# Kernel tuning notes

Hardware: AMD Instinct MI355X
Metric: run time of the kernel (lower is better)

The kernel has to match this reference:

```python
import jax, jax.numpy as jnp
import numpy as np

K = 20
EPS = 1e-5
NEG_SLOPE = 0.2


def knn_idx(feat, k):
    # feat: (B, N, C). Pairwise neg squared distance, top-k nearest (self included).
    inner = jnp.einsum('bnc,bmc->bnm', feat, feat)          # (B,N,N)
    sq = jnp.sum(feat * feat, axis=-1)                      # (B,N)
    pd = 2.0 * inner - sq[:, :, None] - sq[:, None, :]      # -||xi-xj||^2
    return jax.lax.top_k(pd, k)[1]                          # (B,N,k)


def edge_conv(feat, W, g, b, m, v, k):
    # feat: (B,N,C); W: (O, 2C); BN params over O channels (eval-mode BN).
    idx = knn_idx(feat, k)                                  # (B,N,k)
    nbr = jnp.take_along_axis(feat[:, None, :, :], idx[..., None], axis=2)  # (B,N,k,C)
    ctr = jnp.broadcast_to(feat[:, :, None, :], nbr.shape)
    edge = jnp.concatenate([nbr - ctr, ctr], axis=-1)       # (B,N,k,2C)
    h = jnp.einsum('bnkc,oc->bnko', edge, W)                # 1x1 conv
    h = (h - m) * (g / jnp.sqrt(v + EPS)) + b               # BatchNorm2d (eval)
    h = jnp.where(h >= 0, h, NEG_SLOPE * h)                 # LeakyReLU(0.2)
    return jnp.max(h, axis=2)                               # max over k -> (B,N,O)


def setup_inputs() -> dict:
    key = jax.random.key(0)
    ks = jax.random.split(key, 21)
    B, N, C = 4, 4096, 3
    d = {'x': jax.random.normal(ks[0], (B, N, C), dtype=jnp.float32)}
    dims = [(64, 2 * 3), (64, 2 * 64), (128, 2 * 64), (256, 2 * 128)]
    for i, (o, c) in enumerate(dims, start=1):
        j = 1 + (i - 1) * 5
        d[f'W{i}'] = jax.random.normal(ks[j], (o, c), dtype=jnp.float32) * (1.0 / np.sqrt(c))
        d[f'g{i}'] = jax.random.uniform(ks[j + 1], (o,), minval=0.5, maxval=1.5, dtype=jnp.float32)
        d[f'b{i}'] = jax.random.normal(ks[j + 2], (o,), dtype=jnp.float32) * 0.1
        d[f'm{i}'] = jax.random.normal(ks[j + 3], (o,), dtype=jnp.float32) * 0.1
        d[f'v{i}'] = jax.random.uniform(ks[j + 4], (o,), minval=0.5, maxval=1.5, dtype=jnp.float32)
    return d


def reference(x, W1, g1, b1, m1, v1, W2, g2, b2, m2, v2,
              W3, g3, b3, m3, v3, W4, g4, b4, m4, v4):
    x1 = edge_conv(x, W1, g1, b1, m1, v1, K)    # (B,N,64)
    x2 = edge_conv(x1, W2, g2, b2, m2, v2, K)   # (B,N,64)
    x3 = edge_conv(x2, W3, g3, b3, m3, v3, K)   # (B,N,128)
    x4 = edge_conv(x3, W4, g4, b4, m4, v4, K)   # (B,N,256)
    return x4
```

## Files before the change

kernel.cpp:

```cpp
#include <hip/hip_runtime.h>

#define NTOT 4096
#define NBATCH 4
#define KNN 20
#define JSPLIT 8
#define KMRG 28
#define CSLOTM 512

constexpr float NEG_INF = -3.0e38f;

typedef __attribute__((ext_vector_type(8))) short bf16x8;
typedef __attribute__((ext_vector_type(4))) float f32x4;

__device__ __forceinline__ unsigned pk(float f, int j) {
  unsigned u = __float_as_uint(f);
  u = (u & 0x80000000u) ? ~u : (u | 0x80000000u);
  return (u & 0xFFFFF000u) | (unsigned)j;
}

__device__ __forceinline__ void pins8(unsigned u, unsigned (&tv)[8]) {
  if (u > tv[0]) {
    tv[0] = u;
#pragma unroll
    for (int x = 1; x < 8; x++) {
      unsigned mn = min(tv[0], tv[x]);
      unsigned mx = max(tv[0], tv[x]);
      tv[0] = mn;
      tv[x] = mx;
    }
  }
}

__device__ __forceinline__ void gll16(const void* g, void* l) {
  __builtin_amdgcn_global_load_lds(
      (const __attribute__((address_space(1))) unsigned int*)g,
      (__attribute__((address_space(3))) unsigned int*)l, 16, 0, 0);
}

__global__ void prep_w(const float* __restrict__ W, const float* __restrict__ gg,
                       const float* __restrict__ bb, const float* __restrict__ mm,
                       const float* __restrict__ vv, float* __restrict__ Wc,
                       float* __restrict__ bias, int O, int C) {
  int t = blockIdx.x * 256 + threadIdx.x;
  if (t >= 2 * O * C) return;
  int o2 = t / C, c = t - o2 * C;
  int o = (o2 < O) ? o2 : o2 - O;
  float s = gg[o] * rsqrtf(vv[o] + 1e-5f);
  float w = (o2 < O) ? W[o * 2 * C + c] * s
                     : (W[o * 2 * C + C + c] - W[o * 2 * C + c]) * s;
  Wc[o2 * C + c] = w;
  if (o2 >= O && c == 0) bias[o] = bb[o] - mm[o] * s;
}

__global__ void cvt_k(const float* __restrict__ f, ushort* __restrict__ hi,
                      ushort* __restrict__ lo) {
  int p = blockIdx.x * 256 + threadIdx.x;
  float x = f[p];
  unsigned u = __float_as_uint(x);
  unsigned h = (u + 0x7FFFu + ((u >> 16) & 1u)) >> 16;
  float hf = __uint_as_float(h << 16);
  float r = x - hf;
  unsigned v = __float_as_uint(r);
  unsigned l = (v + 0x7FFFu + ((v >> 16) & 1u)) >> 16;
  hi[p] = (ushort)h;
  lo[p] = (ushort)l;
}

__global__ void cvt3_k(const float* __restrict__ f, ushort* __restrict__ hi,
                       ushort* __restrict__ lo) {
  int p = blockIdx.x * 256 + threadIdx.x;
  int pt = p >> 5, dim = p & 31;
  float x = (dim < 3) ? f[pt * 3 + dim] : 0.f;
  unsigned u = __float_as_uint(x);
  unsigned h = (u + 0x7FFFu + ((u >> 16) & 1u)) >> 16;
  float hf = __uint_as_float(h << 16);
  float r = x - hf;
  unsigned v = __float_as_uint(r);
  unsigned l = (v + 0x7FFFu + ((v >> 16) & 1u)) >> 16;
  hi[p] = (ushort)h;
  lo[p] = (ushort)l;
}

template <int C>
__global__ void sqh_k(const float* __restrict__ f, float* __restrict__ sqh) {
  int p = blockIdx.x * 256 + threadIdx.x;
  const float* r = f + (size_t)p * C;
  float s = 0.f;
#pragma unroll
  for (int c4 = 0; c4 < C / 4; c4++) {
    float4 v = *(const float4*)&r[c4 * 4];
    s += v.x * v.x + v.y * v.y + v.z * v.z + v.w * v.w;
  }
  sqh[p] = 0.5f * s;
}

__global__ void sqh3_k(const float* __restrict__ f, float* __restrict__ sqh) {
  int p = blockIdx.x * 256 + threadIdx.x;
  float a = f[(size_t)p * 3 + 0];
  float b2 = f[(size_t)p * 3 + 1];
  float c = f[(size_t)p * 3 + 2];
  sqh[p] = 0.5f * (a * a + b2 * b2 + c * c);
}

template <int C>
__global__ __launch_bounds__(512, 4) void knn_m(const ushort* __restrict__ Xhi,
                                                const ushort* __restrict__ Xlo,
                                                const float* __restrict__ sqh,
                                                unsigned* __restrict__ cval) {
  constexpr int NK = C / 32;
  constexpr int NJT = NTOT / (128 * JSPLIT);
  __shared__ __align__(16) char smem[67584];
  float* sqB = (float*)(smem + 65536);

  int tid = threadIdx.x;
  int raw = blockIdx.x;
  int b = raw & 3;
  int js = (raw >> 3) & (JSPLIT - 1);
  int it = (((raw >> 6) & 15) << 1) | ((raw >> 2) & 1);
  int i0 = it * 128;
  const ushort* xh = Xhi + (size_t)b * NTOT * C;
  const ushort* xl = Xlo + (size_t)b * NTOT * C;

  int l = tid & 63, wid = tid >> 6;
  int wi = wid & 3, wj = wid >> 2;
  int n = l & 15, quad = l >> 4;
  int xr16 = (n & 7) << 4;

  int t0 = l & 1, t1 = (l >> 1) & 1, t2 = (l >> 2) & 1, t3 = (l >> 3) & 1,
      t4 = (l >> 4) & 1, t5 = (l >> 5) & 1;
  int Rl = (t2 ^ t4) | (t3 << 1) | (t4 << 2) | (t5 << 3);
  int ql = (t0 ^ t2 ^ t4) | ((t1 ^ t3) << 1);

  int jbase = js * (NTOT / JSPLIT);

  if (tid < 128) {
    float4 s4 = *(const float4*)&sqh[b * NTOT + jbase + tid * 4];
    *(float4*)&sqB[tid * 4] = s4;
  }
  __syncthreads();

  unsigned tv[2][8];
#pragma unroll
  for (int ti = 0; ti < 2; ti++)
#pragma unroll
    for (int x = 0; x < 8; x++) tv[ti][x] = 0u;

  auto issue = [&](int jtn, int kcn, char* buf) {
    int j0n = jbase + jtn * 128;
    int R = Rl + wid * 16;
    size_t gA = (size_t)(i0 + R) * C + kcn + ql * 8;
    size_t gB = (size_t)(j0n + R) * C + kcn + ql * 8;
    char* ld = buf + wid * 1024;
    gll16(xh + gA, ld);
    gll16(xl + gA, ld + 8192);
    gll16(xh + gB, ld + 16384);
    gll16(xl + gB, ld + 24576);
  };

  issue(0, 0, smem);

  int g = 0;
  for (int jt = 0; jt < NJT; jt++) {
    int j0 = jbase + jt * 128;

    f32x4 acc[4][2];
#pragma unroll
    for (int tj = 0; tj < 4; tj++)
#pragma unroll
      for (int ti = 0; ti < 2; ti++) acc[tj][ti] = (f32x4)(0.f);

    for (int kc = 0; kc < NK; kc++) {
      __builtin_amdgcn_s_barrier();
      int njt = (kc + 1 < NK) ? jt : ((jt + 1 == NJT) ? 0 : jt + 1);
      int nkc = (kc + 1 < NK) ? (kc + 1) * 32 : 0;
      issue(njt, nkc, smem + ((g + 1) & 1) * 32768);
      asm volatile("s_waitcnt vmcnt(4)" ::: "memory");
      __builtin_amdgcn_s_barrier();
      const char* bc = smem + (g & 1) * 32768;

      bf16x8 ah[2], al_[2];
#pragma unroll
      for (int ti = 0; ti < 2; ti++) {
        int row = wi * 32 + ti * 16 + n;
        int off = (row * 64 + quad * 16) ^ xr16;
        ah[ti] = *(const bf16x8*)(bc + off);
        al_[ti] = *(const bf16x8*)(bc + 8192 + off);
      }
#pragma unroll
      for (int tj = 0; tj < 4; tj++) {
        int row = wj * 64 + tj * 16 + n;
        int off = (row * 64 + quad * 16) ^ xr16;
        bf16x8 bh = *(const bf16x8*)(bc + 16384 + off);
        bf16x8 bl = *(const bf16x8*)(bc + 24576 + off);
#pragma unroll
        for (int ti = 0; ti < 2; ti++) {
          acc[tj][ti] = __builtin_amdgcn_mfma_f32_16x16x32_bf16(bh, ah[ti], acc[tj][ti], 0, 0, 0);
          acc[tj][ti] = __builtin_amdgcn_mfma_f32_16x16x32_bf16(bh, al_[ti], acc[tj][ti], 0, 0, 0);
          acc[tj][ti] = __builtin_amdgcn_mfma_f32_16x16x32_bf16(bl, ah[ti], acc[tj][ti], 0, 0, 0);
        }
      }
      g++;
    }

    float4 sq4[4];
#pragma unroll
    for (int tj = 0; tj < 4; tj++)
      sq4[tj] = *(const float4*)&sqB[jt * 128 + wj * 64 + tj * 16 + quad * 4];
#pragma unroll
    for (int ti = 0; ti < 2; ti++) {
#pragma unroll
      for (int tj = 0; tj < 4; tj++) {
        float v0 = acc[tj][ti][0] - sq4[tj].x;
        float v1 = acc[tj][ti][1] - sq4[tj].y;
        float v2 = acc[tj][ti][2] - sq4[tj].z;
        float v3 = acc[tj][ti][3] - sq4[tj].w;
        float m4 = fmaxf(fmaxf(v0, v1), fmaxf(v2, v3));
        if (pk(m4, 0xFFF) > tv[ti][0]) {
          int jb = j0 + wj * 64 + tj * 16 + quad * 4;
          pins8(pk(v0, jb + 0), tv[ti]);
          pins8(pk(v1, jb + 1), tv[ti]);
          pins8(pk(v2, jb + 2), tv[ti]);
          pins8(pk(v3, jb + 3), tv[ti]);
        }
      }
    }
  }

#pragma unroll
  for (int ti = 0; ti < 2; ti++) {
    int p = b * NTOT + i0 + wi * 32 + ti * 16 + n;
    unsigned* dst = cval + (size_t)p * CSLOTM + js * 64 + wj * 32 + quad * 8;
    uint4 o0, o1;
    o0.x = tv[ti][0]; o0.y = tv[ti][1]; o0.z = tv[ti][2]; o0.w = tv[ti][3];
    o1.x = tv[ti][4]; o1.y = tv[ti][5]; o1.z = tv[ti][6]; o1.w = tv[ti][7];
    *(uint4*)&dst[0] = o0;
    *(uint4*)&dst[4] = o1;
  }
}

template <int C, int NC>
__global__ __launch_bounds__(256) void kref_w(const float* __restrict__ feat,
                                              const unsigned* __restrict__ cval,
                                              int* __restrict__ outidx) {
  constexpr int NPL = NC / 64;
  int tid = threadIdx.x;
  int lane = tid & 63;
  int p = blockIdx.x * 4 + (tid >> 6);
  int b = p >> 12;
  int i = p & (NTOT - 1);
  const float* fb = feat + (size_t)b * NTOT * C;

  unsigned c[NPL];
  if constexpr (NPL == 8) {
    uint4 aa = *(const uint4*)&cval[(size_t)p * NC + lane * 8];
    uint4 bb2 = *(const uint4*)&cval[(size_t)p * NC + lane * 8 + 4];
    c[0] = aa.x; c[1] = aa.y; c[2] = aa.z; c[3] = aa.w;
    c[4] = bb2.x; c[5] = bb2.y; c[6] = bb2.z; c[7] = bb2.w;
  } else {
    uint4 aa = *(const uint4*)&cval[(size_t)p * NC + lane * 4];
    c[0] = aa.x; c[1] = aa.y; c[2] = aa.z; c[3] = aa.w;
  }

  int myj = -1;
#pragma unroll
  for (int t = 0; t < KMRG; t++) {
    unsigned m = c[0];
#pragma unroll
    for (int x = 1; x < NPL; x++) m = max(m, c[x]);
#pragma unroll
    for (int s = 1; s < 64; s <<= 1) m = max(m, (unsigned)__shfl_xor((int)m, s));
    if (lane == t) myj = (int)(m & 0xFFFu);
#pragma unroll
    for (int x = 0; x < NPL; x++)
      if (c[x] == m) c[x] = 0;
  }

  float myval = NEG_INF;
  if constexpr (C == 3) {
    if (lane < KMRG) {
      float x0 = fb[(size_t)i * 3 + 0];
      float x1 = fb[(size_t)i * 3 + 1];
      float x2 = fb[(size_t)i * 3 + 2];
      float y0 = fb[(size_t)myj * 3 + 0];
      float y1 = fb[(size_t)myj * 3 + 1];
      float y2 = fb[(size_t)myj * 3 + 2];
      float d0 = x0 - y0, d1 = x1 - y1, d2 = x2 - y2;
      myval = -(d0 * d0 + d1 * d1 + d2 * d2);
    }
  } else {
    constexpr int SL = C / 8;
    int m8 = lane & 7;
    float4 xs[SL / 4];
#pragma unroll
    for (int q4 = 0; q4 < SL / 4; q4++)
      xs[q4] = *(const float4*)&fb[(size_t)i * C + m8 * SL + q4 * 4];
#pragma unroll
    for (int ps = 0; ps < (KMRG + 7) / 8; ps++) {
      int src = ps * 8 + (lane >> 3);
      src = (src < KMRG) ? src : KMRG - 1;
      int j = __shfl(myj, src);
      float d = 0.f;
#pragma unroll
      for (int q4 = 0; q4 < SL / 4; q4++) {
        float4 yv = *(const float4*)&fb[(size_t)j * C + m8 * SL + q4 * 4];
        float dx = xs[q4].x - yv.x;
        float dy = xs[q4].y - yv.y;
        float dz = xs[q4].z - yv.z;
        float dw = xs[q4].w - yv.w;
        d += dx * dx + dy * dy + dz * dz + dw * dw;
      }
#pragma unroll
      for (int s = 1; s < 8; s <<= 1) d += __shfl_xor(d, s);
      float sd = __shfl(d, (lane & 7) << 3);
      bool upd = ((lane >> 3) == ps) && (lane < KMRG);
      myval = upd ? -sd : myval;
    }
  }

#pragma unroll
  for (int k = 2; k <= 64; k <<= 1) {
#pragma unroll
    for (int j2 = k >> 1; j2 > 0; j2 >>= 1) {
      float ov = __shfl_xor(myval, j2);
      int oj = __shfl_xor(myj, j2);
      bool ogt = (ov > myval) || (ov == myval && oj < myj);
      bool lower = ((lane & j2) == 0);
      bool desc = ((lane & k) == 0);
      bool take = (desc == (lower == ogt));
      myval = take ? ov : myval;
      myj = take ? oj : myj;
    }
  }

  if (lane < KNN) outidx[(size_t)p * KNN + lane] = myj;
}

__global__ __launch_bounds__(256) void gemm128(const float* __restrict__ A,
                                               const float* __restrict__ Wc,
                                               const float* __restrict__ bias,
                                               float* __restrict__ Y, int K, int N2,
                                               int O) {
  constexpr int P = 140;
  __shared__ float As[16 * P];
  __shared__ float Bs[16 * P];
  int tid = threadIdx.x;
  int n0 = blockIdx.x * 128;
  int m0 = blockIdx.y * 128;
  int tx = tid & 15, ty = tid >> 4;
  int aoff = (ty * 8) + (((ty * 8) >> 5) << 2);
  int boff = (tx * 8) + (((tx * 8) >> 5) << 2);
  float acc[8][8];
#pragma unroll
  for (int ii = 0; ii < 8; ii++)
#pragma unroll
    for (int jj = 0; jj < 8; jj++) acc[ii][jj] = 0.f;

  for (int kc = 0; kc < K; kc += 16) {
    __syncthreads();
#pragma unroll
    for (int l = 0; l < 2; l++) {
      int e = tid + 256 * l;
      int rr = e >> 2, c4 = e & 3;
      int sc = rr + ((rr >> 5) << 2);
      float4 va = *(const float4*)&A[(size_t)(m0 + rr) * K + kc + c4 * 4];
      As[(c4 * 4 + 0) * P + sc] = va.x;
      As[(c4 * 4 + 1) * P + sc] = va.y;
      As[(c4 * 4 + 2) * P + sc] = va.z;
      As[(c4 * 4 + 3) * P + sc] = va.w;
      float4 vb = *(const float4*)&Wc[(size_t)(n0 + rr) * K + kc + c4 * 4];
      Bs[(c4 * 4 + 0) * P + sc] = vb.x;
      Bs[(c4 * 4 + 1) * P + sc] = vb.y;
      Bs[(c4 * 4 + 2) * P + sc] = vb.z;
      Bs[(c4 * 4 + 3) * P + sc] = vb.w;
    }
    __syncthreads();
#pragma unroll 8
    for (int k = 0; k < 16; k++) {
      float4 a0 = *(const float4*)&As[k * P + aoff];
      float4 a1 = *(const float4*)&As[k * P + aoff + 4];
      float4 b0 = *(const float4*)&Bs[k * P + boff];
      float4 b1 = *(const float4*)&Bs[k * P + boff + 4];
      float av[8] = {a0.x, a0.y, a0.z, a0.w, a1.x, a1.y, a1.z, a1.w};
      float bv[8] = {b0.x, b0.y, b0.z, b0.w, b1.x, b1.y, b1.z, b1.w};
#pragma unroll
      for (int ii = 0; ii < 8; ii++)
#pragma unroll
        for (int jj = 0; jj < 8; jj++)
          acc[ii][jj] = fmaf(av[ii], bv[jj], acc[ii][jj]);
    }
  }

  int col0 = n0 + tx * 8;
  float bv[8];
#pragma unroll
  for (int jj = 0; jj < 8; jj++) {
    int col = col0 + jj;
    bv[jj] = (col >= O) ? bias[col - O] : 0.f;
  }
#pragma unroll
  for (int ii = 0; ii < 8; ii++) {
    int row = m0 + ty * 8 + ii;
    float4 o0, o1;
    o0.x = acc[ii][0] + bv[0];
    o0.y = acc[ii][1] + bv[1];
    o0.z = acc[ii][2] + bv[2];
    o0.w = acc[ii][3] + bv[3];
    o1.x = acc[ii][4] + bv[4];
    o1.y = acc[ii][5] + bv[5];
    o1.z = acc[ii][6] + bv[6];
    o1.w = acc[ii][7] + bv[7];
    *(float4*)&Y[(size_t)row * N2 + col0] = o0;
    *(float4*)&Y[(size_t)row * N2 + col0 + 4] = o1;
  }
}

__global__ __launch_bounds__(256) void gemm_k(const float* __restrict__ A,
                                              const float* __restrict__ Wc,
                                              const float* __restrict__ bias,
                                              float* __restrict__ Y, int K, int N2,
                                              int O) {
  __shared__ float As[8 * 68];
  __shared__ float Bs[8 * 68];
  int tid = threadIdx.x;
  int n0 = blockIdx.x * 64;
  int m0 = blockIdx.y * 64;
  int tx = tid & 15, ty = tid >> 4;
  float acc[4][4] = {};
  for (int k0 = 0; k0 < K; k0 += 8) {
    __syncthreads();
    {
      int e = tid, mm = e >> 3, kk = e & 7;
      As[kk * 68 + mm] = (k0 + kk < K) ? A[(size_t)(m0 + mm) * K + k0 + kk] : 0.f;
      int nn = mm;
      Bs[kk * 68 + nn] = (k0 + kk < K) ? Wc[(size_t)(n0 + nn) * K + k0 + kk] : 0.f;
      e = tid + 256;
      mm = e >> 3;
      kk = e & 7;
      As[kk * 68 + mm] = (k0 + kk < K) ? A[(size_t)(m0 + mm) * K + k0 + kk] : 0.f;
      nn = mm;
      Bs[kk * 68 + nn] = (k0 + kk < K) ? Wc[(size_t)(n0 + nn) * K + k0 + kk] : 0.f;
    }
    __syncthreads();
#pragma unroll
    for (int kk = 0; kk < 8; kk++) {
      float4 av = *(float4*)&As[kk * 68 + ty * 4];
      float4 bv = *(float4*)&Bs[kk * 68 + tx * 4];
      float a[4] = {av.x, av.y, av.z, av.w};
      float bb2[4] = {bv.x, bv.y, bv.z, bv.w};
#pragma unroll
      for (int ii = 0; ii < 4; ii++)
#pragma unroll
        for (int jj = 0; jj < 4; jj++) acc[ii][jj] += a[ii] * bb2[jj];
    }
  }
  int col = n0 + tx * 4;
  bool isV = (col >= O);
  float b0 = 0.f, b1 = 0.f, b2 = 0.f, b3 = 0.f;
  if (isV) {
    b0 = bias[col + 0 - O];
    b1 = bias[col + 1 - O];
    b2 = bias[col + 2 - O];
    b3 = bias[col + 3 - O];
  }
#pragma unroll
  for (int ii = 0; ii < 4; ii++) {
    int row = m0 + ty * 4 + ii;
    float4 o4;
    o4.x = acc[ii][0] + b0;
    o4.y = acc[ii][1] + b1;
    o4.z = acc[ii][2] + b2;
    o4.w = acc[ii][3] + b3;
    *(float4*)&Y[(size_t)row * N2 + col] = o4;
  }
}

template <int O>
__global__ __launch_bounds__(256) void gmax_v(const float* __restrict__ Y,
                                              const int* __restrict__ idx,
                                              float* __restrict__ out) {
  constexpr int T = O / 4;
  constexpr int G = 256 / T;
  int tid = threadIdx.x;
  int p = blockIdx.x * G + tid / T;
  int o4 = (tid % T) * 4;
  int b = p >> 12;
  constexpr int N2 = 2 * O;
  const int* ip = idx + (size_t)p * KNN;
  float4 m = make_float4(NEG_INF, NEG_INF, NEG_INF, NEG_INF);
#pragma unroll
  for (int k = 0; k < KNN; k++) {
    int j = ip[k];
    float4 v = *(const float4*)&Y[((size_t)(b * NTOT + j)) * N2 + o4];
    m.x = fmaxf(m.x, v.x);
    m.y = fmaxf(m.y, v.y);
    m.z = fmaxf(m.z, v.z);
    m.w = fmaxf(m.w, v.w);
  }
  float4 c = *(const float4*)&Y[(size_t)p * N2 + O + o4];
  float4 o;
  o.x = c.x + m.x;
  o.y = c.y + m.y;
  o.z = c.z + m.z;
  o.w = c.w + m.w;
  o.x = (o.x >= 0.f) ? o.x : 0.2f * o.x;
  o.y = (o.y >= 0.f) ? o.y : 0.2f * o.y;
  o.z = (o.z >= 0.f) ? o.z : 0.2f * o.z;
  o.w = (o.w >= 0.f) ? o.w : 0.2f * o.w;
  *(float4*)&out[(size_t)p * O + o4] = o;
}

template <int C, int O>
static void run_layer(const float* fin, void* const* w5, float* fout, float* Wc,
                      float* biasb, int* idx, float* Y, float* sqh,
                      unsigned* cval, ushort* Xhi, ushort* Xlo,
                      hipStream_t stream) {
  const float* W = (const float*)w5[0];
  const float* g = (const float*)w5[1];
  const float* bb = (const float*)w5[2];
  const float* mm = (const float*)w5[3];
  const float* vv = (const float*)w5[4];
  int N2 = 2 * O;
  prep_w<<<(2 * O * C + 255) / 256, 256, 0, stream>>>(W, g, bb, mm, vv, Wc, biasb, O, C);
  if (C == 3) {
    cvt3_k<<<NBATCH * NTOT * 32 / 256, 256, 0, stream>>>(fin, Xhi, Xlo);
    sqh3_k<<<NBATCH * NTOT / 256, 256, 0, stream>>>(fin, sqh);
    knn_m<32><<<NBATCH * 32 * JSPLIT, 512, 0, stream>>>(Xhi, Xlo, sqh, cval);
    kref_w<3, 512><<<NBATCH * NTOT / 4, 256, 0, stream>>>(fin, cval, idx);
    dim3 gg(N2 / 64, NBATCH * NTOT / 64);
    gemm_k<<<gg, 256, 0, stream>>>(fin, Wc, biasb, Y, C, N2, O);
  } else {
    constexpr int CC = (C == 3) ? 64 : C;
    cvt_k<<<NBATCH * NTOT * CC / 256, 256, 0, stream>>>(fin, Xhi, Xlo);
    sqh_k<CC><<<NBATCH * NTOT / 256, 256, 0, stream>>>(fin, sqh);
    knn_m<CC><<<NBATCH * 32 * JSPLIT, 512, 0, stream>>>(Xhi, Xlo, sqh, cval);
    kref_w<CC, 512><<<NBATCH * NTOT / 4, 256, 0, stream>>>(fin, cval, idx);
    dim3 gg(N2 / 128, NBATCH * NTOT / 128);
    gemm128<<<gg, 256, 0, stream>>>(fin, Wc, biasb, Y, C, N2, O);
  }
  gmax_v<O><<<NBATCH * NTOT / (256 / (O / 4)), 256, 0, stream>>>(Y, idx, fout);
}

extern "C" void kernel_launch(void* const* d_in, const int* in_sizes, int n_in,
                              void* d_out, int out_size, void* d_ws, size_t ws_size,
                              hipStream_t stream) {
  const float* x = (const float*)d_in[0];
  char* ws = (char*)d_ws;
  float* Wc = (float*)(ws + 0);
  float* biasb = (float*)(ws + 262144);
  int* idx = (int*)(ws + 263168);
  float* sqh = (float*)(ws + 1573888);
  float* Y = (float*)(ws + 1639424);
  float* x1 = (float*)(ws + 35193856);
  float* x2 = (float*)(ws + 39388160);
  float* x3 = (float*)(ws + 43582464);

  unsigned* cval = (unsigned*)Y;
  ushort* X1h = (ushort*)x1;
  ushort* X1l = X1h + (size_t)NBATCH * NTOT * 32;
  ushort* X2h = (ushort*)x2;
  ushort* X2l = X2h + (size_t)NBATCH * NTOT * 64;
  ushort* X3h = (ushort*)x3;
  ushort* X3l = X3h + (size_t)NBATCH * NTOT * 64;
  float* outf = (float*)d_out;
  ushort* X4h = (ushort*)outf;
  ushort* X4l = X4h + (size_t)NBATCH * NTOT * 128;

  run_layer<3, 64>(x, d_in + 1, x1, Wc, biasb, idx, Y, sqh, cval, X1h, X1l, stream);
  run_layer<64, 64>(x1, d_in + 6, x2, Wc, biasb, idx, Y, sqh, cval, X2h, X2l, stream);
  run_layer<64, 128>(x2, d_in + 11, x3, Wc, biasb, idx, Y, sqh, cval, X3h, X3l, stream);
  run_layer<128, 256>(x3, d_in + 16, outf, Wc, biasb, idx, Y, sqh, cval, X4h, X4l, stream);
}
```

Measured before the change: 673.5 us.

## Halve kNN block count, presort candidate lists, and trim refine count

Each kNN block now walks two adjacent column splits, emitting the per-split top-8 candidates after each, so half as many blocks are launched and each reuses its staged row tile. The refine kernel sorts each lane's 8 candidates with a sorting network so each extraction round is a shift instead of a max over all slots and a compare-clear. The number of candidates refined drops from 28 to 24, removing a partial shuffle pass. The candidate margin for exact top-20 selection is smaller, and fewer blocks may lower GPU occupancy.

```diff
diff --git a/kernel.cpp b/kernel.cpp
--- a/kernel.cpp
+++ b/kernel.cpp
@@ -4,7 +4,7 @@
 #define NBATCH 4
 #define KNN 20
 #define JSPLIT 8
-#define KMRG 28
+#define KMRG 24
 #define CSLOTM 512
 
 constexpr float NEG_INF = -3.0e38f;
@@ -109,15 +109,17 @@
                                                 unsigned* __restrict__ cval) {
   constexpr int NK = C / 32;
   constexpr int NJT = NTOT / (128 * JSPLIT);
-  __shared__ __align__(16) char smem[67584];
+  constexpr int NSQ = 2 * NJT;
+  __shared__ __align__(16) char smem[69632];
   float* sqB = (float*)(smem + 65536);
 
   int tid = threadIdx.x;
   int raw = blockIdx.x;
   int b = raw & 3;
-  int js = (raw >> 3) & (JSPLIT - 1);
-  int it = (((raw >> 6) & 15) << 1) | ((raw >> 2) & 1);
+  int jsp = (raw >> 3) & 3;
+  int it = (((raw >> 5) & 15) << 1) | ((raw >> 2) & 1);
   int i0 = it * 128;
+  int jpbase = jsp * 1024;
   const ushort* xh = Xhi + (size_t)b * NTOT * C;
   const ushort* xl = Xlo + (size_t)b * NTOT * C;
 
@@ -131,10 +133,8 @@
   int Rl = (t2 ^ t4) | (t3 << 1) | (t4 << 2) | (t5 << 3);
   int ql = (t0 ^ t2 ^ t4) | ((t1 ^ t3) << 1);
 
-  int jbase = js * (NTOT / JSPLIT);
-
-  if (tid < 128) {
-    float4 s4 = *(const float4*)&sqh[b * NTOT + jbase + tid * 4];
+  if (tid < 256) {
+    float4 s4 = *(const float4*)&sqh[b * NTOT + jpbase + tid * 4];
     *(float4*)&sqB[tid * 4] = s4;
   }
   __syncthreads();
@@ -145,8 +145,8 @@
 #pragma unroll
     for (int x = 0; x < 8; x++) tv[ti][x] = 0u;
 
-  auto issue = [&](int jtn, int kcn, char* buf) {
-    int j0n = jbase + jtn * 128;
+  auto issue = [&](int sn, int kcn, char* buf) {
+    int j0n = jpbase + sn * 128;
     int R = Rl + wid * 16;
     size_t gA = (size_t)(i0 + R) * C + kcn + ql * 8;
     size_t gB = (size_t)(j0n + R) * C + kcn + ql * 8;
@@ -160,8 +160,8 @@
   issue(0, 0, smem);
 
   int g = 0;
-  for (int jt = 0; jt < NJT; jt++) {
-    int j0 = jbase + jt * 128;
+  for (int s = 0; s < NSQ; s++) {
+    int j0 = jpbase + s * 128;
 
     f32x4 acc[4][2];
 #pragma unroll
@@ -171,9 +171,9 @@
 
     for (int kc = 0; kc < NK; kc++) {
       __builtin_amdgcn_s_barrier();
-      int njt = (kc + 1 < NK) ? jt : ((jt + 1 == NJT) ? 0 : jt + 1);
+      int nsn = (kc + 1 < NK) ? s : ((s + 1 == NSQ) ? 0 : s + 1);
       int nkc = (kc + 1 < NK) ? (kc + 1) * 32 : 0;
-      issue(njt, nkc, smem + ((g + 1) & 1) * 32768);
+      issue(nsn, nkc, smem + ((g + 1) & 1) * 32768);
       asm volatile("s_waitcnt vmcnt(4)" ::: "memory");
       __builtin_amdgcn_s_barrier();
       const char* bc = smem + (g & 1) * 32768;
@@ -205,7 +205,7 @@
     float4 sq4[4];
 #pragma unroll
     for (int tj = 0; tj < 4; tj++)
-      sq4[tj] = *(const float4*)&sqB[jt * 128 + wj * 64 + tj * 16 + quad * 4];
+      sq4[tj] = *(const float4*)&sqB[s * 128 + wj * 64 + tj * 16 + quad * 4];
 #pragma unroll
     for (int ti = 0; ti < 2; ti++) {
 #pragma unroll
@@ -224,17 +224,22 @@
         }
       }
     }
-  }
-
-#pragma unroll
-  for (int ti = 0; ti < 2; ti++) {
-    int p = b * NTOT + i0 + wi * 32 + ti * 16 + n;
-    unsigned* dst = cval + (size_t)p * CSLOTM + js * 64 + wj * 32 + quad * 8;
-    uint4 o0, o1;
-    o0.x = tv[ti][0]; o0.y = tv[ti][1]; o0.z = tv[ti][2]; o0.w = tv[ti][3];
-    o1.x = tv[ti][4]; o1.y = tv[ti][5]; o1.z = tv[ti][6]; o1.w = tv[ti][7];
-    *(uint4*)&dst[0] = o0;
-    *(uint4*)&dst[4] = o1;
+
+    if (s == NJT - 1 || s == NSQ - 1) {
+      int js = jsp * 2 + ((s == NSQ - 1) ? 1 : 0);
+#pragma unroll
+      for (int ti = 0; ti < 2; ti++) {
+        int p = b * NTOT + i0 + wi * 32 + ti * 16 + n;
+        unsigned* dst = cval + (size_t)p * CSLOTM + js * 64 + wj * 32 + quad * 8;
+        uint4 o0, o1;
+        o0.x = tv[ti][0]; o0.y = tv[ti][1]; o0.z = tv[ti][2]; o0.w = tv[ti][3];
+        o1.x = tv[ti][4]; o1.y = tv[ti][5]; o1.z = tv[ti][6]; o1.w = tv[ti][7];
+        *(uint4*)&dst[0] = o0;
+        *(uint4*)&dst[4] = o1;
+#pragma unroll
+        for (int x = 0; x < 8; x++) tv[ti][x] = 0u;
+      }
+    }
   }
 }
 
@@ -242,7 +247,6 @@
 __global__ __launch_bounds__(256) void kref_w(const float* __restrict__ feat,
                                               const unsigned* __restrict__ cval,
                                               int* __restrict__ outidx) {
-  constexpr int NPL = NC / 64;
   int tid = threadIdx.x;
   int lane = tid & 63;
   int p = blockIdx.x * 4 + (tid >> 6);
@@ -250,29 +254,46 @@
   int i = p & (NTOT - 1);
   const float* fb = feat + (size_t)b * NTOT * C;
 
-  unsigned c[NPL];
-  if constexpr (NPL == 8) {
+  unsigned c[8];
+  {
     uint4 aa = *(const uint4*)&cval[(size_t)p * NC + lane * 8];
     uint4 bb2 = *(const uint4*)&cval[(size_t)p * NC + lane * 8 + 4];
     c[0] = aa.x; c[1] = aa.y; c[2] = aa.z; c[3] = aa.w;
     c[4] = bb2.x; c[5] = bb2.y; c[6] = bb2.z; c[7] = bb2.w;
-  } else {
-    uint4 aa = *(const uint4*)&cval[(size_t)p * NC + lane * 4];
-    c[0] = aa.x; c[1] = aa.y; c[2] = aa.z; c[3] = aa.w;
-  }
+  }
+
+#define CE(a, bq)                      \
+  {                                    \
+    unsigned mx = max(c[a], c[bq]);    \
+    unsigned mn = min(c[a], c[bq]);    \
+    c[a] = mx;                         \
+    c[bq] = mn;                        \
+  }
+  CE(0, 1) CE(2, 3) CE(4, 5) CE(6, 7)
+  CE(0, 2) CE(1, 3) CE(4, 6) CE(5, 7)
+  CE(1, 2) CE(5, 6) CE(0, 4) CE(3, 7)
+  CE(1, 5) CE(2, 6)
+  CE(1, 4) CE(3, 6)
+  CE(2, 4) CE(3, 5)
+  CE(3, 4)
+#undef CE
 
   int myj = -1;
 #pragma unroll
   for (int t = 0; t < KMRG; t++) {
     unsigned m = c[0];
 #pragma unroll
-    for (int x = 1; x < NPL; x++) m = max(m, c[x]);
-#pragma unroll
     for (int s = 1; s < 64; s <<= 1) m = max(m, (unsigned)__shfl_xor((int)m, s));
     if (lane == t) myj = (int)(m & 0xFFFu);
-#pragma unroll
-    for (int x = 0; x < NPL; x++)
-      if (c[x] == m) c[x] = 0;
+    bool mine = (c[0] == m);
+    c[0] = mine ? c[1] : c[0];
+    c[1] = mine ? c[2] : c[1];
+    c[2] = mine ? c[3] : c[2];
+    c[3] = mine ? c[4] : c[3];
+    c[4] = mine ? c[5] : c[4];
+    c[5] = mine ? c[6] : c[5];
+    c[6] = mine ? c[7] : c[6];
+    c[7] = mine ? 0u : c[7];
   }
 
   float myval = NEG_INF;
@@ -295,9 +316,8 @@
     for (int q4 = 0; q4 < SL / 4; q4++)
       xs[q4] = *(const float4*)&fb[(size_t)i * C + m8 * SL + q4 * 4];
 #pragma unroll
-    for (int ps = 0; ps < (KMRG + 7) / 8; ps++) {
+    for (int ps = 0; ps < KMRG / 8; ps++) {
       int src = ps * 8 + (lane >> 3);
-      src = (src < KMRG) ? src : KMRG - 1;
       int j = __shfl(myj, src);
       float d = 0.f;
 #pragma unroll
@@ -312,7 +332,7 @@
 #pragma unroll
       for (int s = 1; s < 8; s <<= 1) d += __shfl_xor(d, s);
       float sd = __shfl(d, (lane & 7) << 3);
-      bool upd = ((lane >> 3) == ps) && (lane < KMRG);
+      bool upd = ((lane >> 3) == ps);
       myval = upd ? -sd : myval;
     }
   }
@@ -524,7 +544,7 @@
   if (C == 3) {
     cvt3_k<<<NBATCH * NTOT * 32 / 256, 256, 0, stream>>>(fin, Xhi, Xlo);
     sqh3_k<<<NBATCH * NTOT / 256, 256, 0, stream>>>(fin, sqh);
-    knn_m<32><<<NBATCH * 32 * JSPLIT, 512, 0, stream>>>(Xhi, Xlo, sqh, cval);
+    knn_m<32><<<NBATCH * 32 * (JSPLIT / 2), 512, 0, stream>>>(Xhi, Xlo, sqh, cval);
     kref_w<3, 512><<<NBATCH * NTOT / 4, 256, 0, stream>>>(fin, cval, idx);
     dim3 gg(N2 / 64, NBATCH * NTOT / 64);
     gemm_k<<<gg, 256, 0, stream>>>(fin, Wc, biasb, Y, C, N2, O);
@@ -532,7 +552,7 @@
     constexpr int CC = (C == 3) ? 64 : C;
     cvt_k<<<NBATCH * NTOT * CC / 256, 256, 0, stream>>>(fin, Xhi, Xlo);
     sqh_k<CC><<<NBATCH * NTOT / 256, 256, 0, stream>>>(fin, sqh);
-    knn_m<CC><<<NBATCH * 32 * JSPLIT, 512, 0, stream>>>(Xhi, Xlo, sqh, cval);
+    knn_m<CC><<<NBATCH * 32 * (JSPLIT / 2), 512, 0, stream>>>(Xhi, Xlo, sqh, cval);
     kref_w<CC, 512><<<NBATCH * NTOT / 4, 256, 0, stream>>>(fin, cval, idx);
     dim3 gg(N2 / 128, NBATCH * NTOT / 128);
     gemm128<<<gg, 256, 0, stream>>>(fin, Wc, biasb, Y, C, N2, O);
```

New measurement: 659.9 us. 1.02x faster.
